# Optimization experiments

Measured on AMD Instinct MI355X. Metric: run time of the kernel, lower is better.

## Reference

```python
import jax, jax.numpy as jnp
import numpy as np

EMBED = 512
HEADS = 8
DIM_HEAD = 64
SCALE = DIM_HEAD ** -0.5


def setup_inputs() -> dict:
    key = jax.random.key(0)
    k1, k2, k3 = jax.random.split(key, 3)
    x = jax.random.normal(k1, (1, EMBED, 64, 64), dtype=jnp.float32)
    # nn.Linear(embed, 3*embed) weight [out, in] -> store transposed [in, out] for x @ W
    W_qkv = jax.random.normal(k2, (EMBED, 3 * EMBED), dtype=jnp.float32) * (EMBED ** -0.5)
    b_qkv = jax.random.normal(k3, (3 * EMBED,), dtype=jnp.float32) * 0.01
    return {"x": x, "W_qkv": W_qkv, "b_qkv": b_qkv}


def reference(x, W_qkv, b_qkv):
    B, E, h, w = x.shape
    N = h * w
    # [B, E, H, W] -> [B, N, E]
    xs = x.reshape(B, E, N).transpose(0, 2, 1)
    qkv = xs @ W_qkv + b_qkv                      # [B, N, 3E]
    q, k, v = jnp.split(qkv, 3, axis=-1)          # each [B, N, E]

    def heads(t):
        return t.reshape(B, N, HEADS, DIM_HEAD).transpose(0, 2, 1, 3)  # [B, H, N, dh]

    q, k, v = heads(q), heads(k), heads(v)
    # raw (non-softmax) attention scores, materialized as in the original
    attn = jnp.einsum('bhqd,bhkd->bhqk', q, k) * SCALE  # [B, H, N, N]
    coarse_attn = attn.sum(axis=-2)                     # sum over queries -> [B, H, N]
    output = jnp.einsum('bhqk,bhkd->bhqd', attn, v)     # [B, H, N, dh]
    return coarse_attn, output
```

## Files before the change

### kernel.cpp

```cpp
#include <hip/hip_runtime.h>


#define N_TOK 4096
#define EMBED 512
#define J3    1536
#define HEADS 8
#define DH    64
#define SCALE 0.125f

typedef float  floatx4  __attribute__((ext_vector_type(4)));
typedef short  shortx8  __attribute__((ext_vector_type(8)));
typedef unsigned short ushortx4 __attribute__((ext_vector_type(4)));

__device__ inline unsigned short f2bf(float f) {
    union { float f; unsigned int u; } x; x.f = f;
    unsigned int u = x.u;
    unsigned int r = u + 0x7fffu + ((u >> 16) & 1u);
    return (unsigned short)(r >> 16);
}
__device__ inline float bf2f(unsigned short u) {
    union { unsigned int u; float f; } x; x.u = ((unsigned int)u) << 16; return x.f;
}

__global__ __launch_bounds__(256) void tr_cvt(const float* __restrict__ src,
                                              unsigned short* __restrict__ dst, int C) {
    __shared__ float T[64][65];
    const int c0 = blockIdx.x * 64, r0 = blockIdx.y * 64;
    const int t = threadIdx.x;
    #pragma unroll
    for (int k = 0; k < 16; ++k) {
        int i = t + 256 * k; int r = i >> 6, c = i & 63;
        T[r][c] = src[(size_t)(r0 + r) * C + c0 + c];
    }
    __syncthreads();
    #pragma unroll
    for (int k = 0; k < 16; ++k) {
        int i = t + 256 * k; int cr = i >> 6, cc = i & 63;
        dst[(size_t)(c0 + cr) * 512 + r0 + cc] = f2bf(T[cc][cr]);
    }
}

__global__ __launch_bounds__(256) void qkv_mfma(const unsigned short* __restrict__ xT,
                                                const unsigned short* __restrict__ WT,
                                                const float* __restrict__ bias,
                                                unsigned short* __restrict__ qkv) {
    __shared__ __align__(16) short As[128 * 32];
    __shared__ __align__(16) short Bs[128 * 32];
    const int j0 = blockIdx.x * 128, n0 = blockIdx.y * 128;
    const int t = threadIdx.x, lane = t & 63, w = t >> 6;
    const int wm = w & 1, wn = w >> 1;
    const int quad = lane >> 4, mrow = lane & 15;
    floatx4 acc[4][4] = {};
    for (int e0 = 0; e0 < 512; e0 += 32) {
        __syncthreads();
        #pragma unroll
        for (int s = 0; s < 2; ++s) {
            int i = t + 256 * s;
            int row = i >> 2, q = i & 3;
            shortx8 av = *(const shortx8*)(xT + (size_t)(n0 + row) * 512 + e0 + q * 8);
            shortx8 bv = *(const shortx8*)(WT + (size_t)(j0 + row) * 512 + e0 + q * 8);
            *(shortx8*)&As[row * 32 + q * 8] = av;
            *(shortx8*)&Bs[row * 32 + q * 8] = bv;
        }
        __syncthreads();
        shortx8 a[4], b[4];
        #pragma unroll
        for (int mi = 0; mi < 4; ++mi)
            a[mi] = *(const shortx8*)&As[(wm * 64 + mi * 16 + mrow) * 32 + quad * 8];
        #pragma unroll
        for (int ni = 0; ni < 4; ++ni)
            b[ni] = *(const shortx8*)&Bs[(wn * 64 + ni * 16 + mrow) * 32 + quad * 8];
        #pragma unroll
        for (int mi = 0; mi < 4; ++mi)
            #pragma unroll
            for (int ni = 0; ni < 4; ++ni)
                acc[mi][ni] = __builtin_amdgcn_mfma_f32_16x16x32_bf16(a[mi], b[ni], acc[mi][ni], 0, 0, 0);
    }
    const int col = lane & 15, qr = lane >> 4;
    #pragma unroll
    for (int ni = 0; ni < 4; ++ni) {
        int j = j0 + wn * 64 + ni * 16 + col;
        float bj = bias[j];
        #pragma unroll
        for (int mi = 0; mi < 4; ++mi)
            #pragma unroll
            for (int r = 0; r < 4; ++r) {
                int n = n0 + wm * 64 + mi * 16 + qr * 4 + r;
                qkv[(size_t)n * J3 + j] = f2bf(acc[mi][ni][r] + bj);
            }
    }
}

__global__ __launch_bounds__(256) void kv_partial(const unsigned short* __restrict__ qkv,
                                                  float* __restrict__ Mp, float* __restrict__ qsp) {
    const int h = blockIdx.x, ch = blockIdx.y;
    const int n0 = ch * 128;
    __shared__ __align__(16) float Ks[64][68];
    __shared__ __align__(16) float Vs[64][68];
    __shared__ float qred[256];
    const int t = threadIdx.x;
    const int tx = t & 15, ty = t >> 4;
    float acc[4][4] = {};
    float qa = 0.f;
    for (int st = 0; st < 2; ++st) {
        const int nb = n0 + st * 64;
        __syncthreads();
        #pragma unroll
        for (int k = 0; k < 4; ++k) {
            int i = t + 256 * k; int row = i >> 4, c4 = (i & 15) * 4;
            ushortx4 k4 = *(const ushortx4*)(qkv + (size_t)(nb + row) * J3 + EMBED + h * DH + c4);
            ushortx4 v4 = *(const ushortx4*)(qkv + (size_t)(nb + row) * J3 + 2 * EMBED + h * DH + c4);
            Ks[row][c4 + 0] = bf2f(k4[0]); Ks[row][c4 + 1] = bf2f(k4[1]);
            Ks[row][c4 + 2] = bf2f(k4[2]); Ks[row][c4 + 3] = bf2f(k4[3]);
            Vs[row][c4 + 0] = bf2f(v4[0]); Vs[row][c4 + 1] = bf2f(v4[1]);
            Vs[row][c4 + 2] = bf2f(v4[2]); Vs[row][c4 + 3] = bf2f(v4[3]);
        }
        {
            int d = t & 63, q0 = (t >> 6) * 16;
            for (int n = q0; n < q0 + 16; ++n)
                qa += bf2f(qkv[(size_t)(nb + n) * J3 + h * DH + d]);
        }
        __syncthreads();
        for (int n = 0; n < 64; ++n) {
            floatx4 kf = *(const floatx4*)&Ks[n][ty * 4];
            floatx4 vf = *(const floatx4*)&Vs[n][tx * 4];
            #pragma unroll
            for (int i = 0; i < 4; ++i)
                #pragma unroll
                for (int j = 0; j < 4; ++j)
                    acc[i][j] += kf[i] * vf[j];
        }
    }
    qred[t] = qa;
    __syncthreads();
    float* mp = Mp + ((size_t)h * 32 + ch) * 4096;
    #pragma unroll
    for (int i = 0; i < 4; ++i) {
        floatx4 v = { acc[i][0], acc[i][1], acc[i][2], acc[i][3] };
        *(floatx4*)&mp[(ty * 4 + i) * 64 + tx * 4] = v;
    }
    if (t < 64)
        qsp[((size_t)h * 32 + ch) * 64 + t] = qred[t] + qred[t + 64] + qred[t + 128] + qred[t + 192];
}

__global__ __launch_bounds__(256) void reduce_md(const float* __restrict__ Mp,
                                                 const float* __restrict__ qsp,
                                                 float* __restrict__ M, float* __restrict__ qsum) {
    const int b = blockIdx.x;
    const int h = b >> 2, part = b & 3;
    const int t = threadIdx.x;
    #pragma unroll
    for (int k = 0; k < 4; ++k) {
        int i = part * 1024 + t + 256 * k;
        float s = 0.f;
        for (int c = 0; c < 32; ++c) s += Mp[((size_t)h * 32 + c) * 4096 + i];
        M[h * 4096 + i] = s;
    }
    if (part == 0 && t < 64) {
        float s = 0.f;
        for (int c = 0; c < 32; ++c) s += qsp[((size_t)h * 32 + c) * 64 + t];
        qsum[h * DH + t] = s;
    }
}

__global__ __launch_bounds__(256) void out_kernel(const unsigned short* __restrict__ qkv,
                                                  const float* __restrict__ M,
                                                  const float* __restrict__ qsum,
                                                  float* __restrict__ out) {
    const int h = blockIdx.x, ch = blockIdx.y;
    const int n0 = ch * 64;
    __shared__ __align__(16) float Ms[64][68];
    __shared__ __align__(16) float Qs[64][68];
    __shared__ unsigned short Kb[64][66];
    __shared__ float qs[64];
    __shared__ float cred[256];
    const int t = threadIdx.x;
    #pragma unroll
    for (int k = 0; k < 4; ++k) {
        int i = t + 256 * k; int row = i >> 4, c4 = (i & 15) * 4;
        floatx4 mv = *(const floatx4*)&M[h * 4096 + row * 64 + c4];
        *(floatx4*)&Ms[row][c4] = mv;
        ushortx4 q4 = *(const ushortx4*)(qkv + (size_t)(n0 + row) * J3 + h * DH + c4);
        Qs[row][c4 + 0] = bf2f(q4[0]); Qs[row][c4 + 1] = bf2f(q4[1]);
        Qs[row][c4 + 2] = bf2f(q4[2]); Qs[row][c4 + 3] = bf2f(q4[3]);
    }
    #pragma unroll
    for (int k = 0; k < 16; ++k) {
        int i = t + 256 * k; int row = i >> 6, col = i & 63;
        Kb[row][col] = qkv[(size_t)(n0 + row) * J3 + EMBED + h * DH + col];
    }
    if (t < 64) qs[t] = qsum[h * DH + t];
    __syncthreads();
    const int tx = t & 15, ty = t >> 4;
    float acc[4][4] = {};
    for (int dp = 0; dp < 64; ++dp) {
        floatx4 mf = *(const floatx4*)&Ms[dp][tx * 4];
        float q0 = Qs[ty * 4 + 0][dp], q1 = Qs[ty * 4 + 1][dp];
        float q2 = Qs[ty * 4 + 2][dp], q3 = Qs[ty * 4 + 3][dp];
        #pragma unroll
        for (int j = 0; j < 4; ++j) {
            acc[0][j] += q0 * mf[j]; acc[1][j] += q1 * mf[j];
            acc[2][j] += q2 * mf[j]; acc[3][j] += q3 * mf[j];
        }
    }
    float* op = out + HEADS * N_TOK + (size_t)h * N_TOK * DH;
    #pragma unroll
    for (int i = 0; i < 4; ++i) {
        int n = n0 + ty * 4 + i;
        floatx4 v = { acc[i][0] * SCALE, acc[i][1] * SCALE, acc[i][2] * SCALE, acc[i][3] * SCALE };
        *(floatx4*)&op[(size_t)n * DH + tx * 4] = v;
    }
    {
        int cn = t & 63, part = t >> 6;
        float ca = 0.f;
        for (int dp = part * 16; dp < part * 16 + 16; ++dp)
            ca += bf2f(Kb[cn][dp]) * qs[dp];
        cred[t] = ca;
    }
    __syncthreads();
    if (t < 64)
        out[h * N_TOK + n0 + t] = (cred[t] + cred[t + 64] + cred[t + 128] + cred[t + 192]) * SCALE;
}

extern "C" void kernel_launch(void* const* d_in, const int* in_sizes, int n_in,
                              void* d_out, int out_size, void* d_ws, size_t ws_size,
                              hipStream_t stream) {
    const float* x = (const float*)d_in[0];
    const float* W = (const float*)d_in[1];
    const float* b = (const float*)d_in[2];
    float* out = (float*)d_out;

    unsigned short* xT   = (unsigned short*)d_ws;
    unsigned short* WT   = xT + (size_t)N_TOK * EMBED;
    unsigned short* qkvb = WT + (size_t)J3 * EMBED;
    float* Mp   = (float*)(qkvb + (size_t)N_TOK * J3);
    float* qsp  = Mp + (size_t)HEADS * 32 * 4096;
    float* M    = qsp + (size_t)HEADS * 32 * 64;
    float* qsum = M + (size_t)HEADS * 4096;

    tr_cvt<<<dim3(64, 8), 256, 0, stream>>>(x, xT, N_TOK);
    tr_cvt<<<dim3(24, 8), 256, 0, stream>>>(W, WT, J3);
    qkv_mfma<<<dim3(12, 32), 256, 0, stream>>>(xT, WT, b, qkvb);
    kv_partial<<<dim3(8, 32), 256, 0, stream>>>(qkvb, Mp, qsp);
    reduce_md<<<32, 256, 0, stream>>>(Mp, qsp, M, qsum);
    out_kernel<<<dim3(8, 64), 256, 0, stream>>>(qkvb, M, qsum, out);
}
```

Measured before the change: 117.3 us.

## Merge transpose launches, async LDS loads in QKV GEMM, MFMA output kernel

Folds the two transpose-convert launches into one and vectorizes their bf16 stores. The QKV GEMM now stages tiles with global_load_lds async copies instead of going through registers. kv_partial splits the work into twice as many smaller token chunks. reduce_md writes a transposed bf16 M, so out_kernel can compute Q·M with bf16 MFMA in a single-wave block and do the coarse sum straight from global memory. This aims to cut launch count and scalar FMA work, at the cost of bf16 rounding of M and larger partial buffers.

```diff
diff --git a/kernel.cpp b/kernel.cpp
--- a/kernel.cpp
+++ b/kernel.cpp
@@ -11,21 +11,32 @@
 typedef float  floatx4  __attribute__((ext_vector_type(4)));
 typedef short  shortx8  __attribute__((ext_vector_type(8)));
 typedef unsigned short ushortx4 __attribute__((ext_vector_type(4)));
+typedef unsigned short ushortx2 __attribute__((ext_vector_type(2)));
+typedef unsigned int u32;
 
 __device__ inline unsigned short f2bf(float f) {
-    union { float f; unsigned int u; } x; x.f = f;
-    unsigned int u = x.u;
-    unsigned int r = u + 0x7fffu + ((u >> 16) & 1u);
+    union { float f; u32 u; } x; x.f = f;
+    u32 r = x.u + 0x7fffu + ((x.u >> 16) & 1u);
     return (unsigned short)(r >> 16);
 }
 __device__ inline float bf2f(unsigned short u) {
-    union { unsigned int u; float f; } x; x.u = ((unsigned int)u) << 16; return x.f;
-}
-
-__global__ __launch_bounds__(256) void tr_cvt(const float* __restrict__ src,
-                                              unsigned short* __restrict__ dst, int C) {
+    union { u32 u; float f; } x; x.u = ((u32)u) << 16; return x.f;
+}
+__device__ static inline void async_copy16(void* lds, const void* g) {
+    auto* gp = (const __attribute__((address_space(1))) u32*)g;
+    auto* lp = (__attribute__((address_space(3))) u32*)lds;
+    __builtin_amdgcn_global_load_lds(gp, lp, 16, 0, 0);
+}
+
+__global__ __launch_bounds__(256) void tr_cvt(const float* __restrict__ x,
+                                              const float* __restrict__ W,
+                                              unsigned short* __restrict__ xT,
+                                              unsigned short* __restrict__ WT) {
+    const float* src; unsigned short* dst; int C, bx = blockIdx.x;
+    if (bx < 64) { src = x; dst = xT; C = N_TOK; }
+    else         { src = W; dst = WT; C = J3; bx -= 64; }
     __shared__ float T[64][65];
-    const int c0 = blockIdx.x * 64, r0 = blockIdx.y * 64;
+    const int c0 = bx * 64, r0 = blockIdx.y * 64;
     const int t = threadIdx.x;
     #pragma unroll
     for (int k = 0; k < 16; ++k) {
@@ -34,9 +45,11 @@
     }
     __syncthreads();
     #pragma unroll
-    for (int k = 0; k < 16; ++k) {
-        int i = t + 256 * k; int cr = i >> 6, cc = i & 63;
-        dst[(size_t)(c0 + cr) * 512 + r0 + cc] = f2bf(T[cc][cr]);
+    for (int k = 0; k < 4; ++k) {
+        int i = t + 256 * k; int cr = i >> 4, cc4 = (i & 15) * 4;
+        ushortx4 o = { f2bf(T[cc4 + 0][cr]), f2bf(T[cc4 + 1][cr]),
+                       f2bf(T[cc4 + 2][cr]), f2bf(T[cc4 + 3][cr]) };
+        *(ushortx4*)&dst[(size_t)(c0 + cr) * 512 + r0 + cc4] = o;
     }
 }
 
@@ -57,10 +70,10 @@
         for (int s = 0; s < 2; ++s) {
             int i = t + 256 * s;
             int row = i >> 2, q = i & 3;
-            shortx8 av = *(const shortx8*)(xT + (size_t)(n0 + row) * 512 + e0 + q * 8);
-            shortx8 bv = *(const shortx8*)(WT + (size_t)(j0 + row) * 512 + e0 + q * 8);
-            *(shortx8*)&As[row * 32 + q * 8] = av;
-            *(shortx8*)&Bs[row * 32 + q * 8] = bv;
+            char* abase = (char*)As + (size_t)w * 1024 + (size_t)s * 4096;
+            char* bbase = (char*)Bs + (size_t)w * 1024 + (size_t)s * 4096;
+            async_copy16(abase, xT + (size_t)(n0 + row) * 512 + e0 + q * 8);
+            async_copy16(bbase, WT + (size_t)(j0 + row) * 512 + e0 + q * 8);
         }
         __syncthreads();
         shortx8 a[4], b[4];
@@ -94,132 +107,121 @@
 __global__ __launch_bounds__(256) void kv_partial(const unsigned short* __restrict__ qkv,
                                                   float* __restrict__ Mp, float* __restrict__ qsp) {
     const int h = blockIdx.x, ch = blockIdx.y;
-    const int n0 = ch * 128;
+    const int n0 = ch * 64;
     __shared__ __align__(16) float Ks[64][68];
     __shared__ __align__(16) float Vs[64][68];
     __shared__ float qred[256];
     const int t = threadIdx.x;
+    #pragma unroll
+    for (int k = 0; k < 2; ++k) {
+        int i = t + 256 * k; int row = i >> 3, c8 = (i & 7) * 8;
+        shortx8 k8 = *(const shortx8*)(qkv + (size_t)(n0 + row) * J3 + EMBED + h * DH + c8);
+        shortx8 v8 = *(const shortx8*)(qkv + (size_t)(n0 + row) * J3 + 2 * EMBED + h * DH + c8);
+        #pragma unroll
+        for (int j = 0; j < 8; ++j) {
+            Ks[row][c8 + j] = bf2f((unsigned short)k8[j]);
+            Vs[row][c8 + j] = bf2f((unsigned short)v8[j]);
+        }
+    }
+    {
+        int d = t & 63, q0 = (t >> 6) * 16;
+        float qa = 0.f;
+        for (int n = q0; n < q0 + 16; ++n)
+            qa += bf2f(qkv[(size_t)(n0 + n) * J3 + h * DH + d]);
+        qred[t] = qa;
+    }
+    __syncthreads();
     const int tx = t & 15, ty = t >> 4;
     float acc[4][4] = {};
-    float qa = 0.f;
-    for (int st = 0; st < 2; ++st) {
-        const int nb = n0 + st * 64;
-        __syncthreads();
-        #pragma unroll
-        for (int k = 0; k < 4; ++k) {
-            int i = t + 256 * k; int row = i >> 4, c4 = (i & 15) * 4;
-            ushortx4 k4 = *(const ushortx4*)(qkv + (size_t)(nb + row) * J3 + EMBED + h * DH + c4);
-            ushortx4 v4 = *(const ushortx4*)(qkv + (size_t)(nb + row) * J3 + 2 * EMBED + h * DH + c4);
-            Ks[row][c4 + 0] = bf2f(k4[0]); Ks[row][c4 + 1] = bf2f(k4[1]);
-            Ks[row][c4 + 2] = bf2f(k4[2]); Ks[row][c4 + 3] = bf2f(k4[3]);
-            Vs[row][c4 + 0] = bf2f(v4[0]); Vs[row][c4 + 1] = bf2f(v4[1]);
-            Vs[row][c4 + 2] = bf2f(v4[2]); Vs[row][c4 + 3] = bf2f(v4[3]);
-        }
-        {
-            int d = t & 63, q0 = (t >> 6) * 16;
-            for (int n = q0; n < q0 + 16; ++n)
-                qa += bf2f(qkv[(size_t)(nb + n) * J3 + h * DH + d]);
-        }
-        __syncthreads();
-        for (int n = 0; n < 64; ++n) {
-            floatx4 kf = *(const floatx4*)&Ks[n][ty * 4];
-            floatx4 vf = *(const floatx4*)&Vs[n][tx * 4];
-            #pragma unroll
-            for (int i = 0; i < 4; ++i)
-                #pragma unroll
-                for (int j = 0; j < 4; ++j)
-                    acc[i][j] += kf[i] * vf[j];
-        }
-    }
-    qred[t] = qa;
-    __syncthreads();
-    float* mp = Mp + ((size_t)h * 32 + ch) * 4096;
+    for (int n = 0; n < 64; ++n) {
+        floatx4 kf = *(const floatx4*)&Ks[n][ty * 4];
+        floatx4 vf = *(const floatx4*)&Vs[n][tx * 4];
+        #pragma unroll
+        for (int i = 0; i < 4; ++i)
+            #pragma unroll
+            for (int j = 0; j < 4; ++j)
+                acc[i][j] += kf[i] * vf[j];
+    }
+    float* mp = Mp + ((size_t)h * 64 + ch) * 4096;
     #pragma unroll
     for (int i = 0; i < 4; ++i) {
         floatx4 v = { acc[i][0], acc[i][1], acc[i][2], acc[i][3] };
         *(floatx4*)&mp[(ty * 4 + i) * 64 + tx * 4] = v;
     }
     if (t < 64)
-        qsp[((size_t)h * 32 + ch) * 64 + t] = qred[t] + qred[t + 64] + qred[t + 128] + qred[t + 192];
+        qsp[((size_t)h * 64 + ch) * 64 + t] = qred[t] + qred[t + 64] + qred[t + 128] + qred[t + 192];
 }
 
 __global__ __launch_bounds__(256) void reduce_md(const float* __restrict__ Mp,
                                                  const float* __restrict__ qsp,
-                                                 float* __restrict__ M, float* __restrict__ qsum) {
-    const int b = blockIdx.x;
-    const int h = b >> 2, part = b & 3;
+                                                 unsigned short* __restrict__ Mt,
+                                                 float* __restrict__ qsum) {
+    const int h = blockIdx.x, part = blockIdx.y;
     const int t = threadIdx.x;
-    #pragma unroll
-    for (int k = 0; k < 4; ++k) {
-        int i = part * 1024 + t + 256 * k;
-        float s = 0.f;
-        for (int c = 0; c < 32; ++c) s += Mp[((size_t)h * 32 + c) * 4096 + i];
-        M[h * 4096 + i] = s;
+    __shared__ float Msh[16][68];
+    const int i0 = part * 1024 + t * 4;
+    floatx4 s = {0.f, 0.f, 0.f, 0.f};
+    #pragma unroll 4
+    for (int c = 0; c < 64; ++c)
+        s += *(const floatx4*)&Mp[((size_t)h * 64 + c) * 4096 + i0];
+    const int dpl = t >> 4, d0 = (t & 15) * 4;
+    *(floatx4*)&Msh[dpl][d0] = s;
+    __syncthreads();
+    {
+        int d = t >> 2, dpl0 = (t & 3) * 4;
+        ushortx4 o = { f2bf(Msh[dpl0 + 0][d]), f2bf(Msh[dpl0 + 1][d]),
+                       f2bf(Msh[dpl0 + 2][d]), f2bf(Msh[dpl0 + 3][d]) };
+        *(ushortx4*)&Mt[(size_t)h * 4096 + d * 64 + part * 16 + dpl0] = o;
     }
     if (part == 0 && t < 64) {
-        float s = 0.f;
-        for (int c = 0; c < 32; ++c) s += qsp[((size_t)h * 32 + c) * 64 + t];
-        qsum[h * DH + t] = s;
-    }
-}
-
-__global__ __launch_bounds__(256) void out_kernel(const unsigned short* __restrict__ qkv,
-                                                  const float* __restrict__ M,
-                                                  const float* __restrict__ qsum,
-                                                  float* __restrict__ out) {
-    const int h = blockIdx.x, ch = blockIdx.y;
-    const int n0 = ch * 64;
-    __shared__ __align__(16) float Ms[64][68];
-    __shared__ __align__(16) float Qs[64][68];
-    __shared__ unsigned short Kb[64][66];
-    __shared__ float qs[64];
-    __shared__ float cred[256];
-    const int t = threadIdx.x;
-    #pragma unroll
-    for (int k = 0; k < 4; ++k) {
-        int i = t + 256 * k; int row = i >> 4, c4 = (i & 15) * 4;
-        floatx4 mv = *(const floatx4*)&M[h * 4096 + row * 64 + c4];
-        *(floatx4*)&Ms[row][c4] = mv;
-        ushortx4 q4 = *(const ushortx4*)(qkv + (size_t)(n0 + row) * J3 + h * DH + c4);
-        Qs[row][c4 + 0] = bf2f(q4[0]); Qs[row][c4 + 1] = bf2f(q4[1]);
-        Qs[row][c4 + 2] = bf2f(q4[2]); Qs[row][c4 + 3] = bf2f(q4[3]);
-    }
-    #pragma unroll
-    for (int k = 0; k < 16; ++k) {
-        int i = t + 256 * k; int row = i >> 6, col = i & 63;
-        Kb[row][col] = qkv[(size_t)(n0 + row) * J3 + EMBED + h * DH + col];
-    }
-    if (t < 64) qs[t] = qsum[h * DH + t];
-    __syncthreads();
-    const int tx = t & 15, ty = t >> 4;
-    float acc[4][4] = {};
-    for (int dp = 0; dp < 64; ++dp) {
-        floatx4 mf = *(const floatx4*)&Ms[dp][tx * 4];
-        float q0 = Qs[ty * 4 + 0][dp], q1 = Qs[ty * 4 + 1][dp];
-        float q2 = Qs[ty * 4 + 2][dp], q3 = Qs[ty * 4 + 3][dp];
-        #pragma unroll
-        for (int j = 0; j < 4; ++j) {
-            acc[0][j] += q0 * mf[j]; acc[1][j] += q1 * mf[j];
-            acc[2][j] += q2 * mf[j]; acc[3][j] += q3 * mf[j];
+        float q = 0.f;
+        for (int c = 0; c < 64; ++c) q += qsp[((size_t)h * 64 + c) * 64 + t];
+        qsum[h * DH + t] = q;
+    }
+}
+
+__global__ __launch_bounds__(64) void out_kernel(const unsigned short* __restrict__ qkv,
+                                                 const unsigned short* __restrict__ Mt,
+                                                 const float* __restrict__ qsum,
+                                                 float* __restrict__ out) {
+    const int h = blockIdx.x, n0 = blockIdx.y * 64;
+    const int lane = threadIdx.x;
+    const int quad = lane >> 4, mrow = lane & 15;
+    floatx4 acc[4][4] = {};
+    #pragma unroll
+    for (int ks = 0; ks < 2; ++ks) {
+        shortx8 a[4], b[4];
+        #pragma unroll
+        for (int mi = 0; mi < 4; ++mi)
+            a[mi] = *(const shortx8*)(qkv + (size_t)(n0 + mi * 16 + mrow) * J3 + h * DH + ks * 32 + quad * 8);
+        #pragma unroll
+        for (int ni = 0; ni < 4; ++ni)
+            b[ni] = *(const shortx8*)(Mt + (size_t)h * 4096 + (ni * 16 + mrow) * 64 + ks * 32 + quad * 8);
+        #pragma unroll
+        for (int mi = 0; mi < 4; ++mi)
+            #pragma unroll
+            for (int ni = 0; ni < 4; ++ni)
+                acc[mi][ni] = __builtin_amdgcn_mfma_f32_16x16x32_bf16(a[mi], b[ni], acc[mi][ni], 0, 0, 0);
+    }
+    float* op = out + HEADS * N_TOK + (size_t)h * N_TOK * DH;
+    #pragma unroll
+    for (int mi = 0; mi < 4; ++mi)
+        #pragma unroll
+        for (int r = 0; r < 4; ++r) {
+            int n = n0 + mi * 16 + quad * 4 + r;
+            #pragma unroll
+            for (int ni = 0; ni < 4; ++ni)
+                op[(size_t)n * DH + ni * 16 + mrow] = acc[mi][ni][r] * SCALE;
         }
-    }
-    float* op = out + HEADS * N_TOK + (size_t)h * N_TOK * DH;
-    #pragma unroll
-    for (int i = 0; i < 4; ++i) {
-        int n = n0 + ty * 4 + i;
-        floatx4 v = { acc[i][0] * SCALE, acc[i][1] * SCALE, acc[i][2] * SCALE, acc[i][3] * SCALE };
-        *(floatx4*)&op[(size_t)n * DH + tx * 4] = v;
-    }
-    {
-        int cn = t & 63, part = t >> 6;
-        float ca = 0.f;
-        for (int dp = part * 16; dp < part * 16 + 16; ++dp)
-            ca += bf2f(Kb[cn][dp]) * qs[dp];
-        cred[t] = ca;
-    }
-    __syncthreads();
-    if (t < 64)
-        out[h * N_TOK + n0 + t] = (cred[t] + cred[t + 64] + cred[t + 128] + cred[t + 192]) * SCALE;
+    float ca = 0.f;
+    #pragma unroll
+    for (int g = 0; g < 8; ++g) {
+        shortx8 kk = *(const shortx8*)(qkv + (size_t)(n0 + lane) * J3 + EMBED + h * DH + g * 8);
+        #pragma unroll
+        for (int j = 0; j < 8; ++j)
+            ca += bf2f((unsigned short)kk[j]) * qsum[h * DH + g * 8 + j];
+    }
+    out[h * N_TOK + n0 + lane] = ca * SCALE;
 }
 
 extern "C" void kernel_launch(void* const* d_in, const int* in_sizes, int n_in,
@@ -233,15 +235,14 @@
     unsigned short* xT   = (unsigned short*)d_ws;
     unsigned short* WT   = xT + (size_t)N_TOK * EMBED;
     unsigned short* qkvb = WT + (size_t)J3 * EMBED;
-    float* Mp   = (float*)(qkvb + (size_t)N_TOK * J3);
-    float* qsp  = Mp + (size_t)HEADS * 32 * 4096;
-    float* M    = qsp + (size_t)HEADS * 32 * 64;
-    float* qsum = M + (size_t)HEADS * 4096;
-
-    tr_cvt<<<dim3(64, 8), 256, 0, stream>>>(x, xT, N_TOK);
-    tr_cvt<<<dim3(24, 8), 256, 0, stream>>>(W, WT, J3);
+    unsigned short* Mt   = qkvb + (size_t)N_TOK * J3;
+    float* Mp   = (float*)(Mt + (size_t)HEADS * DH * DH);
+    float* qsp  = Mp + (size_t)HEADS * 64 * 4096;
+    float* qsum = qsp + (size_t)HEADS * 64 * 64;
+
+    tr_cvt<<<dim3(88, 8), 256, 0, stream>>>(x, W, xT, WT);
     qkv_mfma<<<dim3(12, 32), 256, 0, stream>>>(xT, WT, b, qkvb);
-    kv_partial<<<dim3(8, 32), 256, 0, stream>>>(qkvb, Mp, qsp);
-    reduce_md<<<32, 256, 0, stream>>>(Mp, qsp, M, qsum);
-    out_kernel<<<dim3(8, 64), 256, 0, stream>>>(qkvb, M, qsum, out);
-}
+    kv_partial<<<dim3(8, 64), 256, 0, stream>>>(qkvb, Mp, qsp);
+    reduce_md<<<dim3(8, 4), 256, 0, stream>>>(Mp, qsp, Mt, qsum);
+    out_kernel<<<dim3(8, 64), 64, 0, stream>>>(qkvb, Mt, qsum, out);
+}
```

New measurement: 107.4 us. 1.09x faster.
